# Optimization experiments

Measured on AMD Instinct MI355X. Metric: run time of the kernel, lower is better.

The kernel has to match this reference:

```python
import jax, jax.numpy as jnp
from jax import lax
import numpy as np

V, E, L, B = 50257, 512, 2048, 8
BASE_RATIO, MIN_RATIO = 0.5, 0.1

def next_power_of_two(x):
    return 1 if x == 0 else 2 ** ((x - 1).bit_length())

def setup_inputs() -> dict:
    key = jax.random.key(0)
    ks = jax.random.split(key, 9)
    s = 0.02
    return {
        "x": jax.random.randint(ks[0], (B, L), 0, V),
        "Wtok": jax.random.normal(ks[1], (V, E), jnp.float32) * s,
        "Wpos": jax.random.normal(ks[2], (L, E), jnp.float32) * s,
        "Wc1": jax.random.normal(ks[3], (3, E, E), jnp.float32) * s,  # WIO layout
        "bc1": jnp.zeros((E,), jnp.float32),
        "Wc2": jax.random.normal(ks[4], (3, E, E), jnp.float32) * s,
        "bc2": jnp.zeros((E,), jnp.float32),
        "Wp": jax.random.normal(ks[5], (E, E), jnp.float32) * (1.0 / np.sqrt(E)),  # torch Linear weight [out,in]
        "bp": jnp.zeros((E,), jnp.float32),
    }

def _conv1d(h, W, b):
    # h: [B, L, E] (NWC), W: [k, in, out] (WIO), SAME padding == torch padding=1 for k=3
    y = lax.conv_general_dilated(h, W, (1,), "SAME", dimension_numbers=("NWC", "WIO", "NWC"))
    return jax.nn.relu(y + b)

def reference(x, Wtok, Wpos, Wc1, bc1, Wc2, bc2, Wp, bp):
    Bsz, Ls = x.shape
    # token + position embedding
    h = Wtok[x] + Wpos[jnp.arange(Ls)][None, :, :]          # [B, L, E]
    h = _conv1d(h, Wc1, bc1)
    h = _conv1d(h, Wc2, bc2)
    # pad to next power of two along sequence
    P = next_power_of_two(Ls)
    if P > Ls:
        h = jnp.pad(h, ((0, 0), (0, P - Ls), (0, 0)))
    x_fft = jnp.fft.fft(h, axis=1)                          # [B, P, E] complex64
    mag = jnp.abs(x_fft)
    thr = 0.1 * mag.max(axis=1, keepdims=True)
    complexity = (mag > thr).astype(jnp.float32).mean(axis=(1, 2))   # [B]
    ratio = jnp.clip(BASE_RATIO * (1.0 - complexity), MIN_RATIO, 1.0)
    N = jnp.clip((ratio * Ls).astype(jnp.int32), 1, Ls)     # [B] kept freq count
    # vectorized equivalent of the per-sample truncation loop:
    # keep first N[i] frequencies (zero the rest), then ifft with n=Ls
    fmask = jnp.arange(Ls)[None, :] < N[:, None]            # [B, L] bool
    x_fft_c = jnp.where(fmask[:, :, None], x_fft[:, :Ls, :], 0.0)
    x_ifft = jnp.fft.ifft(x_fft_c, n=Ls, axis=1).real.astype(h.dtype)  # [B, L, E]
    out = x_ifft @ Wp.T + bp                                # proj
    # recon_target is the exact same computation in the original module
    recon_target = out
    mask_f = fmask.astype(out.dtype)[:, :, None]            # [B, L, 1]
    diff = jnp.abs(out - recon_target) * mask_f
    denom = mask_f.sum() * E
    loss_recon = diff.sum() / jnp.maximum(denom, 1.0)
    return out, loss_recon
```

## Files before the change

### kernel.cpp

```cpp
#include <hip/hip_runtime.h>
#include <hip/hip_bf16.h>
#include <cstddef>

#define BB 8
#define LL 2048
#define EE 512
#define KCONV 1536
#define LPAD 2050

typedef _Float16 h16;
typedef _Float16 h16x2 __attribute__((ext_vector_type(2)));
typedef _Float16 h16x4 __attribute__((ext_vector_type(4)));
typedef _Float16 h16x8 __attribute__((ext_vector_type(8)));
typedef float    f32x4 __attribute__((ext_vector_type(4)));

static const size_t OFF_WT1  = 0;
static const size_t OFF_WT2  = 1572864;
static const size_t OFF_WPB  = 3145728;
static const size_t OFF_CNT2 = 3670016;
static const size_t OFF_H0P  = 4194304;
static const size_t OFF_H1P  = 20987904;
static const size_t OFF_H2T  = 37781504;
static const size_t OFF_XF   = 4194304;
static const size_t OFF_H3E  = 54558720;
static const size_t OFF_H3T  = 20987904;
static const size_t WS_NEED  = 71335936;

__device__ __forceinline__ int padi(int i) { return i + (i >> 5); }
__device__ __forceinline__ int dr5(int n) {
    return ((n & 3) << 8) | (((n >> 2) & 3) << 6) | (((n >> 4) & 3) << 4)
         | (((n >> 6) & 3) << 2) | ((n >> 8) & 3);
}
#define TWOPI_2048 0.0030679616f

__global__ __launch_bounds__(256) void prep_embed_kernel(
    const float* __restrict__ Wc1, const float* __restrict__ Wc2,
    const float* __restrict__ Wp,
    h16* __restrict__ Wt1, h16* __restrict__ Wt2, h16* __restrict__ Wpb,
    const int* __restrict__ x, const float* __restrict__ Wtok,
    const float* __restrict__ Wpos, h16* __restrict__ h0p, h16* __restrict__ h1p)
{
    int blk = blockIdx.x, t = threadIdx.x;
    __shared__ float tl[64][65];
    if (blk < 384) {
        const float* src = (blk < 192) ? Wc1 : Wc2;
        h16* dst = (blk < 192) ? Wt1 : Wt2;
        int tile = blk % 192;
        int o0 = (tile / 24) * 64, r0 = (tile % 24) * 64;
        #pragma unroll
        for (int it = 0; it < 4; ++it) {
            int idx = it * 256 + t;
            int rr = idx >> 4, oo4 = (idx & 15) * 4;
            f32x4 v = *(const f32x4*)(src + (size_t)(r0 + rr) * 512 + o0 + oo4);
            tl[rr][oo4] = v[0]; tl[rr][oo4 + 1] = v[1];
            tl[rr][oo4 + 2] = v[2]; tl[rr][oo4 + 3] = v[3];
        }
        __syncthreads();
        #pragma unroll
        for (int it = 0; it < 4; ++it) {
            int idx = it * 256 + t;
            int oo = idx & 63, rr4 = (idx >> 6) * 4;
            h16x4 v;
            v.x = (h16)tl[rr4][oo]; v.y = (h16)tl[rr4 + 1][oo];
            v.z = (h16)tl[rr4 + 2][oo]; v.w = (h16)tl[rr4 + 3][oo];
            *(h16x4*)(dst + (size_t)(o0 + oo) * 1536 + r0 + rr4) = v;
        }
    } else if (blk < 448) {
        int base = (blk - 384) * 4096;
        #pragma unroll
        for (int i = 0; i < 4; ++i) {
            int idx = base + (i * 256 + t) * 4;
            f32x4 a = *(const f32x4*)(Wp + idx);
            h16x4 v; v.x = (h16)a[0]; v.y = (h16)a[1]; v.z = (h16)a[2]; v.w = (h16)a[3];
            *(h16x4*)(Wpb + idx) = v;
        }
    } else {
        int rowg = (blk - 448) * 4 + (t >> 6);
        int b = rowg / LPAD, r = rowg % LPAD;
        int lane = t & 63;
        size_t o = (size_t)rowg * 512 + lane * 8;
        if (r == 0 || r == LPAD - 1) {
            h16x8 z;
            #pragma unroll
            for (int j = 0; j < 8; ++j) z[j] = (h16)0.f;
            *(h16x8*)(h0p + o) = z;
            *(h16x8*)(h1p + o) = z;
        } else {
            int l = r - 1;
            int tok = x[b * LL + l];
            const f32x4* wt = (const f32x4*)(Wtok + (size_t)tok * 512 + lane * 8);
            const f32x4* wp = (const f32x4*)(Wpos + (size_t)l * 512 + lane * 8);
            f32x4 a0 = wt[0], a1 = wt[1], p0 = wp[0], p1 = wp[1];
            h16x8 v;
            #pragma unroll
            for (int j = 0; j < 4; ++j) v[j] = (h16)(a0[j] + p0[j]);
            #pragma unroll
            for (int j = 0; j < 4; ++j) v[4 + j] = (h16)(a1[j] + p1[j]);
            *(h16x8*)(h0p + o) = v;
        }
    }
}

template<int KTOT, bool RELU, bool TRANSOUT, typename OT>
__global__ __launch_bounds__(512) void gemm3_kernel(
    const h16* __restrict__ A, int a_extra,
    const h16* __restrict__ Bt, const float* __restrict__ bias,
    OT* __restrict__ out, int out_extra, int out_off,
    float* __restrict__ tail)
{
    extern __shared__ __align__(16) h16 lds[];
    const int NKT = KTOT / 64;

    int t = threadIdx.x;
    int w = t >> 6, ln = t & 63;
    int mt = blockIdx.x, nt = blockIdx.y;
    int b = mt >> 3;
    const h16* Ab = A + (size_t)mt * (256 * 512) + (size_t)b * a_extra;
    const h16* Bb = Bt + (size_t)nt * 128 * KTOT;

    int srow = t >> 3;
    int scol = (t & 7) * 8;
    int wr = (w >> 1) * 64, wc = (w & 1) * 64;
    int fr = ln & 15, fg = (ln >> 4) * 8;

    f32x4 acc[4][4];
    #pragma unroll
    for (int m = 0; m < 4; ++m)
        #pragma unroll
        for (int n = 0; n < 4; ++n) acc[m][n] = {0.f, 0.f, 0.f, 0.f};

#define STAGE3(KT, BUF)                                                          \
    {                                                                            \
        int k0_ = (KT) * 64;                                                     \
        h16* sa_ = lds + (BUF) * 16384;                                          \
        h16* sb_ = lds + 49152 + (BUF) * 8192;                                   \
        _Pragma("unroll")                                                        \
        for (int q = 0; q < 4; ++q) {                                            \
            int row_ = q * 64 + srow;                                            \
            int sc_ = scol ^ ((row_ & 7) << 3);                                  \
            __builtin_amdgcn_global_load_lds(                                    \
                (const __attribute__((address_space(1))) unsigned int*)(Ab + (size_t)row_ * 512 + k0_ + sc_), \
                (__attribute__((address_space(3))) unsigned int*)(sa_ + row_ * 64 + scol), \
                16, 0, 0);                                                       \
        }                                                                        \
        _Pragma("unroll")                                                        \
        for (int q = 0; q < 2; ++q) {                                            \
            int row_ = q * 64 + srow;                                            \
            int sc_ = scol ^ ((row_ & 7) << 3);                                  \
            __builtin_amdgcn_global_load_lds(                                    \
                (const __attribute__((address_space(1))) unsigned int*)(Bb + (size_t)row_ * KTOT + k0_ + sc_), \
                (__attribute__((address_space(3))) unsigned int*)(sb_ + row_ * 64 + scol), \
                16, 0, 0);                                                       \
        }                                                                        \
    }

    STAGE3(0, 0);
    STAGE3(1, 1);
    asm volatile("s_waitcnt vmcnt(6)" ::: "memory");
    __builtin_amdgcn_s_barrier();
    __builtin_amdgcn_sched_barrier(0);

    int c = 0;
    for (int kt = 0; kt < NKT; ++kt) {
        int c2 = c + 2; if (c2 >= 3) c2 -= 3;
        if (kt + 2 < NKT) STAGE3(kt + 2, c2);
        const h16* sa = lds + c * 16384;
        const h16* sb = lds + 49152 + c * 8192;
        #pragma unroll
        for (int kk = 0; kk < 64; kk += 32) {
            h16x8 af[4], bf[4];
            #pragma unroll
            for (int m = 0; m < 4; ++m) {
                int arow = wr + m * 16 + fr;
                af[m] = *(const h16x8*)(sa + arow * 64 + ((kk + fg) ^ ((arow & 7) << 3)));
            }
            #pragma unroll
            for (int n = 0; n < 4; ++n) {
                int brow = wc + n * 16 + fr;
                bf[n] = *(const h16x8*)(sb + brow * 64 + ((kk + fg) ^ ((brow & 7) << 3)));
            }
            __builtin_amdgcn_s_setprio(1);
            #pragma unroll
            for (int m = 0; m < 4; ++m)
                #pragma unroll
                for (int n = 0; n < 4; ++n)
                    acc[m][n] = __builtin_amdgcn_mfma_f32_16x16x32_f16(af[m], bf[n], acc[m][n], 0, 0, 0);
            __builtin_amdgcn_s_setprio(0);
        }
        if (kt + 1 < NKT) {
            if (kt + 2 < NKT) { asm volatile("s_waitcnt vmcnt(6)" ::: "memory"); }
            else              { asm volatile("s_waitcnt vmcnt(0)" ::: "memory"); }
            __builtin_amdgcn_s_barrier();
            __builtin_amdgcn_sched_barrier(0);
        }
        c = c + 1; if (c >= 3) c -= 3;
    }
#undef STAGE3

    int fq = (ln >> 4) * 4;
    if constexpr (TRANSOUT) {
        int mtl = (mt & 7) * 256;
        #pragma unroll
        for (int n = 0; n < 4; ++n) {
            int col = nt * 128 + wc + n * 16 + fr;
            float bv = bias[col];
            #pragma unroll
            for (int m = 0; m < 4; ++m) {
                h16x4 hv;
                #pragma unroll
                for (int r = 0; r < 4; ++r) {
                    float xv = acc[m][n][r] + bv;
                    if (RELU) xv = fmaxf(xv, 0.f);
                    hv[r] = (h16)xv;
                }
                int l0a = mtl + wr + m * 16 + fq;
                *(h16x4*)((h16*)out + ((size_t)(b * 512 + col)) * 2048 + l0a) = hv;
            }
        }
    } else {
        #pragma unroll
        for (int n = 0; n < 4; ++n) {
            int col = nt * 128 + wc + n * 16 + fr;
            float bv = bias[col];
            #pragma unroll
            for (int m = 0; m < 4; ++m) {
                #pragma unroll
                for (int r = 0; r < 4; ++r) {
                    int grow = wr + m * 16 + fq + r;
                    float v = acc[m][n][r] + bv;
                    if (RELU) v = fmaxf(v, 0.f);
                    size_t oi = (size_t)(mt * 256 + grow) * 512 + (size_t)b * out_extra + out_off + col;
                    out[oi] = (OT)v;
                }
            }
        }
    }
    if (tail && mt == 0 && nt == 0 && t == 0) tail[0] = 0.f;
}

__global__ __launch_bounds__(256) void fft_fwd_kernel(
    const h16* __restrict__ h2t, h16x2* __restrict__ Xf, int* __restrict__ cnt2)
{
    __shared__ float sre[1056], sim[1056];
    __shared__ float red[4]; __shared__ int redc[4];
    int t = threadIdx.x;
    int b = blockIdx.x >> 9, e = blockIdx.x & 511;
    const h16* src = h2t + ((size_t)b * 512 + e) * 2048;
    #pragma unroll
    for (int j = 0; j < 2; ++j) {
        int n0 = j * 512 + t * 2;
        h16x4 v = *(const h16x4*)(src + n0 * 2);
        int d0 = padi(dr5(n0)), d1 = padi(dr5(n0 + 1));
        sre[d0] = (float)v.x; sim[d0] = (float)v.y;
        sre[d1] = (float)v.z; sim[d1] = (float)v.w;
    }
    __syncthreads();
    #pragma unroll
    for (int s = 0; s < 5; ++s) {
        int L = 1 << (2 * s);
        int K = 512 >> (2 * s);
        int p = t & (L - 1);
        int base = (t >> (2 * s)) * 4 * L + p;
        float th = (float)(p * K) * TWOPI_2048;
        float s1, c1;
        __sincosf(th, &s1, &c1);
        float c2 = 1.f - 2.f * s1 * s1, s2 = 2.f * s1 * c1;
        float c3 = c1 * c2 - s1 * s2,  s3 = s1 * c2 + c1 * s2;
        int i0 = padi(base), i1 = padi(base + L), i2 = padi(base + 2 * L), i3 = padi(base + 3 * L);
        float x0r = sre[i0], x0i = sim[i0];
        float x1r = sre[i1], x1i = sim[i1];
        float x2r = sre[i2], x2i = sim[i2];
        float x3r = sre[i3], x3i = sim[i3];
        float t1r = x1r * c1 + x1i * s1, t1i = x1i * c1 - x1r * s1;
        float t2r = x2r * c2 + x2i * s2, t2i = x2i * c2 - x2r * s2;
        float t3r = x3r * c3 + x3i * s3, t3i = x3i * c3 - x3r * s3;
        float ar = x0r + t2r, ai = x0i + t2i;
        float cr = x0r - t2r, ci = x0i - t2i;
        float br_ = t1r + t3r, bi_ = t1i + t3i;
        float dr_ = t1r - t3r, di_ = t1i - t3i;
        sre[i0] = ar + br_; sim[i0] = ai + bi_;
        sre[i2] = ar - br_; sim[i2] = ai - bi_;
        sre[i1] = cr + di_; sim[i1] = ci - dr_;
        sre[i3] = cr - di_; sim[i3] = ci + dr_;
        __syncthreads();
    }
    size_t xb = ((size_t)b * 512 + e) * 1024;
    float m_a, m_b, m_c, m_d, m_e = 0.f;
    {
        int k = t;
        int km = (1024 - k) & 1023;
        float vkr = sre[padi(k)],  vki = sim[padi(k)];
        float vmr = sre[padi(km)], vmi = sim[padi(km)];
        float p2r = 0.5f * (vkr + vmr), p2i = 0.5f * (vki - vmi);
        float gr  = 0.5f * (vkr - vmr), gi  = 0.5f * (vki + vmi);
        float sn, c;
        __sincosf((float)k * TWOPI_2048, &sn, &c);
        float rr = gr * c + gi * sn, ri = gi * c - gr * sn;
        float x0r = p2r + ri, x0i = p2i - rr;
        float x1r = p2r - ri, x1i = -p2i - rr;
        h16x2 o0; o0.x = (h16)x0r; o0.y = (h16)x0i;
        Xf[xb + k] = o0;
        m_a = sqrtf(x0r * x0r + x0i * x0i);
        m_b = sqrtf(x1r * x1r + x1i * x1i);
        if (k != 0) { h16x2 o1; o1.x = (h16)x1r; o1.y = (h16)x1i; Xf[xb + 1024 - k] = o1; }
    }
    {
        int k = t + 256;
        int km = 1024 - k;
        float vkr = sre[padi(k)],  vki = sim[padi(k)];
        float vmr = sre[padi(km)], vmi = sim[padi(km)];
        float p2r = 0.5f * (vkr + vmr), p2i = 0.5f * (vki - vmi);
        float gr  = 0.5f * (vkr - vmr), gi  = 0.5f * (vki + vmi);
        float sn, c;
        __sincosf((float)k * TWOPI_2048, &sn, &c);
        float rr = gr * c + gi * sn, ri = gi * c - gr * sn;
        float x0r = p2r + ri, x0i = p2i - rr;
        float x1r = p2r - ri, x1i = -p2i - rr;
        h16x2 o0; o0.x = (h16)x0r; o0.y = (h16)x0i;
        Xf[xb + k] = o0;
        h16x2 o1; o1.x = (h16)x1r; o1.y = (h16)x1i;
        Xf[xb + 1024 - k] = o1;
        m_c = sqrtf(x0r * x0r + x0i * x0i);
        m_d = sqrtf(x1r * x1r + x1i * x1i);
    }
    if (t == 0) {
        float vr = sre[padi(512)], vi = sim[padi(512)];
        h16x2 o; o.x = (h16)vr; o.y = (h16)(-vi);
        Xf[xb + 512] = o;
        m_e = sqrtf(vr * vr + vi * vi);
    }
    float lmax = fmaxf(fmaxf(fmaxf(m_a, m_b), fmaxf(m_c, m_d)), m_e);
    #pragma unroll
    for (int off = 32; off; off >>= 1) lmax = fmaxf(lmax, __shfl_xor(lmax, off));
    if ((t & 63) == 0) red[t >> 6] = lmax;
    __syncthreads();
    float thr = 0.1f * fmaxf(fmaxf(red[0], red[1]), fmaxf(red[2], red[3]));
    int wa = (t == 0) ? 1 : 2;
    int c = wa * ((m_a > thr) ? 1 : 0) + wa * ((m_b > thr) ? 1 : 0)
          + 2 * ((m_c > thr) ? 1 : 0) + 2 * ((m_d > thr) ? 1 : 0)
          + 2 * ((m_e > thr) ? 1 : 0);
    #pragma unroll
    for (int off = 32; off; off >>= 1) c += __shfl_xor(c, off);
    if ((t & 63) == 0) redc[t >> 6] = c;
    __syncthreads();
    if (t == 0) cnt2[blockIdx.x] = redc[0] + redc[1] + redc[2] + redc[3];
}

__global__ __launch_bounds__(256) void ifft_kernel(
    const h16x2* __restrict__ Xf, const int* __restrict__ cnt2, h16* __restrict__ h3e)
{
    __shared__ float sre[1056], sim[1056];
    __shared__ int redc[4];
    int t = threadIdx.x;
    int b = blockIdx.x >> 9, e = blockIdx.x & 511;
    int cA = cnt2[b * 512 + t] + cnt2[b * 512 + 256 + t];
    #pragma unroll
    for (int off = 32; off; off >>= 1) cA += __shfl_xor(cA, off);
    if ((t & 63) == 0) redc[t >> 6] = cA;
    __syncthreads();
    int Nb;
    {
        int tot = redc[0] + redc[1] + redc[2] + redc[3];
        float cc = (float)tot * (1.0f / 1048576.0f);
        float ratio = 0.5f * (1.f - cc);
        ratio = fminf(fmaxf(ratio, 0.1f), 1.f);
        int n = (int)(ratio * 2048.f);
        Nb = n < 1 ? 1 : (n > 2048 ? 2048 : n);
    }
    size_t xb = ((size_t)b * 512 + e) * 1024;
    #pragma unroll
    for (int j = 0; j < 2; ++j) {
        int k0 = j * 512 + 2 * t;
        h16x4 v = *(const h16x4*)((const h16*)(Xf + xb + k0));
        bool kp0 = k0 < Nb, kp1 = (k0 + 1) < Nb;
        float sc0 = (k0 == 0) ? (1.0f / 2048.0f) : (1.0f / 4096.0f);
        int p0 = padi(k0), p1 = padi(k0 + 1);
        sre[p0] = kp0 ? (float)v.x * sc0 : 0.f;
        sim[p0] = kp0 ? (float)v.y * sc0 : 0.f;
        sre[p1] = kp1 ? (float)v.z * (1.0f / 4096.0f) : 0.f;
        sim[p1] = kp1 ? (float)v.w * (1.0f / 4096.0f) : 0.f;
    }
    __syncthreads();
    float u0r, u0i, u0pr = 0.f, u0pi = 0.f, u1r, u1i, u1pr, u1pi, u2r = 0.f, u2i = 0.f;
    {
        int k = t;
        if (k == 0) {
            float wr = sre[padi(0)], wi = sim[padi(0)];
            u0r = wr - wi; u0i = wi + wr;
        } else {
            int km = 1024 - k;
            float akr = sre[padi(k)],  aki = sim[padi(k)];
            float bkr = sre[padi(km)], bki = sim[padi(km)];
            float pr = akr + bkr, pi = aki - bki;
            float gr = akr - bkr, gi = aki + bki;
            float sn, c;
            __sincosf((float)k * TWOPI_2048, &sn, &c);
            float qr = gr * c - gi * sn, qi = gi * c + gr * sn;
            u0r = pr - qi; u0i = pi + qr;
            u0pr = pr + qi; u0pi = qr - pi;
        }
    }
    {
        int k = t + 256;
        int km = 1024 - k;
        float akr = sre[padi(k)],  aki = sim[padi(k)];
        float bkr = sre[padi(km)], bki = sim[padi(km)];
        float pr = akr + bkr, pi = aki - bki;
        float gr = akr - bkr, gi = aki + bki;
        float sn, c;
        __sincosf((float)k * TWOPI_2048, &sn, &c);
        float qr = gr * c - gi * sn, qi = gi * c + gr * sn;
        u1r = pr - qi; u1i = pi + qr;
        u1pr = pr + qi; u1pi = qr - pi;
    }
    if (t == 0) {
        float ar = sre[padi(512)], ai = sim[padi(512)];
        u2r = 2.f * ar; u2i = -2.f * ai;
    }
    __syncthreads();
    {
        int d = padi(dr5(t)); sre[d] = u0r; sim[d] = u0i;
        if (t != 0) { int dp = padi(dr5(1024 - t)); sre[dp] = u0pr; sim[dp] = u0pi; }
        int d1 = padi(dr5(t + 256)); sre[d1] = u1r; sim[d1] = u1i;
        int dp1 = padi(dr5(768 - t)); sre[dp1] = u1pr; sim[dp1] = u1pi;
        if (t == 0) { int d2 = padi(dr5(512)); sre[d2] = u2r; sim[d2] = u2i; }
    }
    __syncthreads();
    #pragma unroll
    for (int s = 0; s < 5; ++s) {
        int L = 1 << (2 * s);
        int K = 512 >> (2 * s);
        int p = t & (L - 1);
        int base = (t >> (2 * s)) * 4 * L + p;
        float th = (float)(p * K) * TWOPI_2048;
        float s1, c1;
        __sincosf(th, &s1, &c1);
        float c2 = 1.f - 2.f * s1 * s1, s2 = 2.f * s1 * c1;
        float c3 = c1 * c2 - s1 * s2,  s3 = s1 * c2 + c1 * s2;
        int i0 = padi(base), i1 = padi(base + L), i2 = padi(base + 2 * L), i3 = padi(base + 3 * L);
        float x0r = sre[i0], x0i = sim[i0];
        float x1r = sre[i1], x1i = sim[i1];
        float x2r = sre[i2], x2i = sim[i2];
        float x3r = sre[i3], x3i = sim[i3];
        float t1r = x1r * c1 - x1i * s1, t1i = x1i * c1 + x1r * s1;
        float t2r = x2r * c2 - x2i * s2, t2i = x2i * c2 + x2r * s2;
        float t3r = x3r * c3 - x3i * s3, t3i = x3i * c3 + x3r * s3;
        float ar = x0r + t2r, ai = x0i + t2i;
        float cr = x0r - t2r, ci = x0i - t2i;
        float br_ = t1r + t3r, bi_ = t1i + t3i;
        float dr_ = t1r - t3r, di_ = t1i - t3i;
        sre[i0] = ar + br_; sim[i0] = ai + bi_;
        sre[i2] = ar - br_; sim[i2] = ai - bi_;
        sre[i1] = cr - di_; sim[i1] = ci + dr_;
        sre[i3] = cr + di_; sim[i3] = ci - dr_;
        __syncthreads();
    }
    h16x2* drow = (h16x2*)(h3e + ((size_t)b * 512 + e) * 2048);
    #pragma unroll
    for (int j = 0; j < 4; ++j) {
        int n = j * 256 + t;
        h16x2 o; o.x = (h16)sre[padi(n)]; o.y = (h16)sim[padi(n)];
        drow[n] = o;
    }
}

__global__ __launch_bounds__(256) void trans_kernel(
    const h16* __restrict__ h3e, h16* __restrict__ h3t)
{
    __shared__ h16 tl[64][68];
    int t = threadIdx.x;
    int blk = blockIdx.x;
    int b = blk >> 8, r = blk & 255;
    int e0 = (r >> 5) * 64, l0 = (r & 31) * 64;
    #pragma unroll
    for (int it = 0; it < 4; ++it) {
        int idx = it * 256 + t;
        int er = idx >> 4, lc = (idx & 15) * 4;
        h16x4 v = *(const h16x4*)(h3e + ((size_t)(b * 512 + e0 + er)) * 2048 + l0 + lc);
        tl[er][lc] = v.x; tl[er][lc + 1] = v.y; tl[er][lc + 2] = v.z; tl[er][lc + 3] = v.w;
    }
    __syncthreads();
    #pragma unroll
    for (int it = 0; it < 4; ++it) {
        int idx = it * 256 + t;
        int lr = idx >> 4, ec = (idx & 15) * 4;
        h16x4 v;
        v.x = tl[ec][lr]; v.y = tl[ec + 1][lr]; v.z = tl[ec + 2][lr]; v.w = tl[ec + 3][lr];
        *(h16x4*)(h3t + ((size_t)(b * 2048 + l0 + lr)) * 512 + e0 + ec) = v;
    }
}

extern "C" void kernel_launch(void* const* d_in, const int* in_sizes, int n_in,
                              void* d_out, int out_size, void* d_ws, size_t ws_size,
                              hipStream_t stream)
{
    const int*   x    = (const int*)d_in[0];
    const float* Wtok = (const float*)d_in[1];
    const float* Wpos = (const float*)d_in[2];
    const float* Wc1  = (const float*)d_in[3];
    const float* bc1  = (const float*)d_in[4];
    const float* Wc2  = (const float*)d_in[5];
    const float* bc2  = (const float*)d_in[6];
    const float* Wp   = (const float*)d_in[7];
    const float* bp   = (const float*)d_in[8];
    float* out = (float*)d_out;

    char* ws = (char*)d_ws;
    if (ws_size < WS_NEED) {
        hipMemsetAsync(d_out, 0xFF, 4, stream);
        return;
    }
    h16*   Wt1  = (h16*)(ws + OFF_WT1);
    h16*   Wt2  = (h16*)(ws + OFF_WT2);
    h16*   Wpb  = (h16*)(ws + OFF_WPB);
    int*   cnt2 = (int*)(ws + OFF_CNT2);
    h16*   h0p  = (h16*)(ws + OFF_H0P);
    h16*   h1p  = (h16*)(ws + OFF_H1P);
    h16*   h2t  = (h16*)(ws + OFF_H2T);
    h16x2* Xf   = (h16x2*)(ws + OFF_XF);
    h16*   h3e  = (h16*)(ws + OFF_H3E);
    h16*   h3t  = (h16*)(ws + OFF_H3T);

    const int GEMM_LDS = 3 * (256 * 64 + 128 * 64) * (int)sizeof(h16);

    hipFuncSetAttribute((const void*)&gemm3_kernel<KCONV, true, false, h16>,
                        hipFuncAttributeMaxDynamicSharedMemorySize, GEMM_LDS);
    hipFuncSetAttribute((const void*)&gemm3_kernel<KCONV, true, true, h16>,
                        hipFuncAttributeMaxDynamicSharedMemorySize, GEMM_LDS);
    hipFuncSetAttribute((const void*)&gemm3_kernel<512, false, false, float>,
                        hipFuncAttributeMaxDynamicSharedMemorySize, GEMM_LDS);

    prep_embed_kernel<<<4548, 256, 0, stream>>>(
        Wc1, Wc2, Wp, Wt1, Wt2, Wpb, x, Wtok, Wpos, h0p, h1p);
    gemm3_kernel<KCONV, true, false, h16><<<dim3(64, 4), 512, GEMM_LDS, stream>>>(
        h0p, 1024, Wt1, bc1, h1p, 1024, 512, nullptr);
    gemm3_kernel<KCONV, true, true, h16><<<dim3(64, 4), 512, GEMM_LDS, stream>>>(
        h1p, 1024, Wt2, bc2, h2t, 0, 0, nullptr);
    fft_fwd_kernel<<<4096, 256, 0, stream>>>(h2t, Xf, cnt2);
    ifft_kernel<<<4096, 256, 0, stream>>>(Xf, cnt2, h3e);
    trans_kernel<<<2048, 256, 0, stream>>>(h3e, h3t);
    gemm3_kernel<512, false, false, float><<<dim3(64, 4), 512, GEMM_LDS, stream>>>(
        h3t, 0, Wpb, bp, out, 0, 0, out + (size_t)BB * LL * EE);
}
```

Measured before the change: 131.1 us.

## Load GEMM A operand straight into registers and keep only B tiles in LDS

The A tile is no longer staged through LDS. Each wave loads its A fragments directly from global memory into registers, double-buffered across k-steps, and only the B tile stays in a triple-buffered LDS ring. This shrinks LDS from 144KB to 48KB, which removes the dynamic shared memory attribute calls and may let more blocks run per CU, and it halves the k-loop unroll structure. The cost is more global traffic, because A rows are reloaded by the two waves that share a row range. It also adds register pressure and uncoalesced-ish 16B global loads whose latency may not be hidden.

```diff
diff --git a/kernel.cpp b/kernel.cpp
--- a/kernel.cpp
+++ b/kernel.cpp
@@ -132,17 +132,7 @@
 #define STAGE3(KT, BUF)                                                          \
     {                                                                            \
         int k0_ = (KT) * 64;                                                     \
-        h16* sa_ = lds + (BUF) * 16384;                                          \
-        h16* sb_ = lds + 49152 + (BUF) * 8192;                                   \
-        _Pragma("unroll")                                                        \
-        for (int q = 0; q < 4; ++q) {                                            \
-            int row_ = q * 64 + srow;                                            \
-            int sc_ = scol ^ ((row_ & 7) << 3);                                  \
-            __builtin_amdgcn_global_load_lds(                                    \
-                (const __attribute__((address_space(1))) unsigned int*)(Ab + (size_t)row_ * 512 + k0_ + sc_), \
-                (__attribute__((address_space(3))) unsigned int*)(sa_ + row_ * 64 + scol), \
-                16, 0, 0);                                                       \
-        }                                                                        \
+        h16* sb_ = lds + (BUF) * 8192;                                           \
         _Pragma("unroll")                                                        \
         for (int q = 0; q < 2; ++q) {                                            \
             int row_ = q * 64 + srow;                                            \
@@ -154,48 +144,67 @@
         }                                                                        \
     }
 
+#define ALOAD(KT, AF)                                                            \
+    {                                                                            \
+        int k0_ = (KT) * 64;                                                     \
+        _Pragma("unroll")                                                        \
+        for (int kk2 = 0; kk2 < 2; ++kk2)                                        \
+            _Pragma("unroll")                                                    \
+            for (int m = 0; m < 4; ++m)                                          \
+                AF[kk2][m] = *(const h16x8*)(Ab + (size_t)(wr + m * 16 + fr) * 512 + k0_ + kk2 * 32 + fg); \
+    }
+
+#define MFMA_TILE(BUF, AF)                                                       \
+    {                                                                            \
+        const h16* sb = lds + (BUF) * 8192;                                      \
+        _Pragma("unroll")                                                        \
+        for (int kk2 = 0; kk2 < 2; ++kk2) {                                      \
+            h16x8 bf[4];                                                         \
+            _Pragma("unroll")                                                    \
+            for (int n = 0; n < 4; ++n) {                                        \
+                int brow = wc + n * 16 + fr;                                     \
+                bf[n] = *(const h16x8*)(sb + brow * 64 + ((kk2 * 32 + fg) ^ ((brow & 7) << 3))); \
+            }                                                                    \
+            __builtin_amdgcn_s_setprio(1);                                       \
+            _Pragma("unroll")                                                    \
+            for (int m = 0; m < 4; ++m)                                          \
+                _Pragma("unroll")                                                \
+                for (int n = 0; n < 4; ++n)                                      \
+                    acc[m][n] = __builtin_amdgcn_mfma_f32_16x16x32_f16(AF[kk2][m], bf[n], acc[m][n], 0, 0, 0); \
+            __builtin_amdgcn_s_setprio(0);                                       \
+        }                                                                        \
+    }
+
+    h16x8 afA[2][4], afB[2][4];
+
     STAGE3(0, 0);
     STAGE3(1, 1);
-    asm volatile("s_waitcnt vmcnt(6)" ::: "memory");
+    __builtin_amdgcn_sched_barrier(0);
+    ALOAD(0, afA);
+    __builtin_amdgcn_sched_barrier(0);
+    asm volatile("s_waitcnt vmcnt(10)" ::: "memory");
     __builtin_amdgcn_s_barrier();
     __builtin_amdgcn_sched_barrier(0);
 
-    int c = 0;
-    for (int kt = 0; kt < NKT; ++kt) {
-        int c2 = c + 2; if (c2 >= 3) c2 -= 3;
-        if (kt + 2 < NKT) STAGE3(kt + 2, c2);
-        const h16* sa = lds + c * 16384;
-        const h16* sb = lds + 49152 + c * 8192;
-        #pragma unroll
-        for (int kk = 0; kk < 64; kk += 32) {
-            h16x8 af[4], bf[4];
-            #pragma unroll
-            for (int m = 0; m < 4; ++m) {
-                int arow = wr + m * 16 + fr;
-                af[m] = *(const h16x8*)(sa + arow * 64 + ((kk + fg) ^ ((arow & 7) << 3)));
-            }
-            #pragma unroll
-            for (int n = 0; n < 4; ++n) {
-                int brow = wc + n * 16 + fr;
-                bf[n] = *(const h16x8*)(sb + brow * 64 + ((kk + fg) ^ ((brow & 7) << 3)));
-            }
-            __builtin_amdgcn_s_setprio(1);
-            #pragma unroll
-            for (int m = 0; m < 4; ++m)
-                #pragma unroll
-                for (int n = 0; n < 4; ++n)
-                    acc[m][n] = __builtin_amdgcn_mfma_f32_16x16x32_f16(af[m], bf[n], acc[m][n], 0, 0, 0);
-            __builtin_amdgcn_s_setprio(0);
-        }
-        if (kt + 1 < NKT) {
-            if (kt + 2 < NKT) { asm volatile("s_waitcnt vmcnt(6)" ::: "memory"); }
-            else              { asm volatile("s_waitcnt vmcnt(0)" ::: "memory"); }
+    for (int kt = 0; kt < NKT; kt += 2) {
+        if (kt + 2 < NKT) STAGE3(kt + 2, (kt + 2) % 3);
+        if (kt + 1 < NKT) ALOAD(kt + 1, afB);
+        MFMA_TILE(kt % 3, afA);
+        __builtin_amdgcn_sched_barrier(0);
+        __builtin_amdgcn_s_barrier();
+        __builtin_amdgcn_sched_barrier(0);
+        if (kt + 3 < NKT) STAGE3(kt + 3, (kt + 3) % 3);
+        if (kt + 2 < NKT) ALOAD(kt + 2, afA);
+        MFMA_TILE((kt + 1) % 3, afB);
+        if (kt + 2 < NKT) {
+            __builtin_amdgcn_sched_barrier(0);
             __builtin_amdgcn_s_barrier();
             __builtin_amdgcn_sched_barrier(0);
         }
-        c = c + 1; if (c >= 3) c -= 3;
     }
 #undef STAGE3
+#undef ALOAD
+#undef MFMA_TILE
 
     int fq = (ln >> 4) * 4;
     if constexpr (TRANSOUT) {
@@ -521,14 +530,7 @@
     h16*   h3e  = (h16*)(ws + OFF_H3E);
     h16*   h3t  = (h16*)(ws + OFF_H3T);
 
-    const int GEMM_LDS = 3 * (256 * 64 + 128 * 64) * (int)sizeof(h16);
-
-    hipFuncSetAttribute((const void*)&gemm3_kernel<KCONV, true, false, h16>,
-                        hipFuncAttributeMaxDynamicSharedMemorySize, GEMM_LDS);
-    hipFuncSetAttribute((const void*)&gemm3_kernel<KCONV, true, true, h16>,
-                        hipFuncAttributeMaxDynamicSharedMemorySize, GEMM_LDS);
-    hipFuncSetAttribute((const void*)&gemm3_kernel<512, false, false, float>,
-                        hipFuncAttributeMaxDynamicSharedMemorySize, GEMM_LDS);
+    const int GEMM_LDS = 3 * (128 * 64) * (int)sizeof(h16);
 
     prep_embed_kernel<<<4548, 256, 0, stream>>>(
         Wc1, Wc2, Wp, Wt1, Wt2, Wpb, x, Wtok, Wpos, h0p, h1p);
```

After: 199.2 us. 52.0% more time.
